# Performance work log

Hardware: AMD Instinct MI355X
Metric: run time of the kernel (lower is better)

## Reference

```python
import jax, jax.numpy as jnp
import numpy as np

B, S, D = 8, 4096, 1024
CAPACITY = 0.75
K = max(1, int(S * CAPACITY))  # 3072


def setup_inputs() -> dict:
    key = jax.random.key(0)
    k1, k2, k3 = jax.random.split(key, 3)
    x = jax.random.normal(k1, (B, S, D), dtype=jnp.float32)
    processed = jax.random.normal(k2, (B, K, D), dtype=jnp.float32)
    w_router = jax.random.normal(k3, (D,), dtype=jnp.float32) * 0.02
    return {"x": x, "processed": processed, "w_router": w_router}


def reference(x, processed, w_router):
    # --- MoDRouter.forward ---
    bsz, seq_len, dim = x.shape
    k = processed.shape[1]
    # scores: (B, S) = Linear(dim -> 1, no bias)
    scores = jnp.einsum('bsd,d->bs', x, w_router)
    # top-k per batch row, sorted descending (matches torch.topk sorted=True)
    topk_scores, indices = jax.lax.top_k(scores, k)  # (B, K)
    # gather routed tokens: (B, K, D)
    routed_x = jnp.take_along_axis(x, indices[:, :, None], axis=1)
    # --- MoDRouter.scatter_back (processed = block output for routed tokens) ---
    weights = jax.nn.softmax(topk_scores, axis=1)[:, :, None]  # (B, K, 1)
    # original values at routed positions == routed_x (same gather)
    blended = processed * weights + (1.0 - weights) * routed_x  # (B, K, D)
    batch_idx = jnp.arange(bsz)[:, None]  # (B, 1)
    output = x.at[batch_idx, indices].set(blended)  # unrouted positions keep x
    return output
```

## Files before the change

### kernel.cpp

```cpp
#include <hip/hip_runtime.h>
#include <math.h>

#define BB 8
#define SS 4096
#define DD 1024
#define KK 3072
#define NCHUNK 8
#define CHUNK 512
#define NELEM (BB * SS)

typedef unsigned long long u64;
typedef unsigned int u32;

__global__ __launch_bounds__(256) void mod_scores(const float* __restrict__ x,
                                                  const float* __restrict__ w,
                                                  float* __restrict__ scores,
                                                  u64* __restrict__ keys) {
    int wave = (int)((blockIdx.x * blockDim.x + threadIdx.x) >> 6);
    int lane = threadIdx.x & 63;
    if (wave >= NELEM) return;
    const float4* xr = (const float4*)(x + (size_t)wave * DD);
    const float4* wr = (const float4*)w;
    float acc = 0.f;
#pragma unroll
    for (int i = 0; i < 4; ++i) {
        float4 a = xr[lane + 64 * i];
        float4 b = wr[lane + 64 * i];
        acc += a.x * b.x + a.y * b.y + a.z * b.z + a.w * b.w;
    }
#pragma unroll
    for (int off = 32; off > 0; off >>= 1)
        acc += __shfl_down(acc, off, 64);
    if (lane == 0) {
        scores[wave] = acc;
        u32 u = __float_as_uint(acc);
        u32 m = (u & 0x80000000u) ? ~u : (u | 0x80000000u);
        keys[wave] = ((u64)(~m) << 32) | (u32)(wave & (SS - 1));
    }
}

__global__ __launch_bounds__(256) void mod_rank_partial(const u64* __restrict__ keys,
                                                        int* __restrict__ pcnt) {
    __shared__ __align__(16) u64 lk[CHUNK];
    const int ob = blockIdx.x / NCHUNK;
    const int c  = blockIdx.x - ob * NCHUNK;
    const int tid = threadIdx.x;
    const int gid = ob * 256 + tid;
    const int b = gid >> 12;
    const int lane = tid & 63;

    const u64* __restrict__ cand = keys + ((size_t)b << 12) + c * CHUNK;
    *(ulonglong2*)&lk[tid * 2] = *(const ulonglong2*)&cand[tid * 2];
    __syncthreads();

    const u64 my = keys[gid];
    const u32 my_hi = (u32)(my >> 32);
    const u32 my_lo = (u32)my;

    int v_cnt = 0;
#pragma unroll
    for (int g = 0; g < 8; ++g) {
        u64 mj[8];
#pragma unroll
        for (int j = 0; j < 8; ++j) {
            u32 h = (u32)__builtin_amdgcn_readlane((int)my_hi, g * 8 + j);
            u32 l = (u32)__builtin_amdgcn_readlane((int)my_lo, g * 8 + j);
            mj[j] = ((u64)h << 32) | l;
        }
        int cnt[8] = {0, 0, 0, 0, 0, 0, 0, 0};
#pragma unroll
        for (int cg = 0; cg < CHUNK / 64; ++cg) {
            u64 cv = lk[cg * 64 + lane];
#pragma unroll
            for (int j = 0; j < 8; ++j)
                cnt[j] += (int)__popcll(__ballot(cv < mj[j]));
        }
#pragma unroll
        for (int j = 0; j < 8; ++j)
            v_cnt = (lane == g * 8 + j) ? cnt[j] : v_cnt;
    }
    pcnt[c * NELEM + gid] = v_cnt;
}

__global__ __launch_bounds__(256) void mod_finalize(const int* __restrict__ pcnt,
                                                    const float* __restrict__ scores,
                                                    int* __restrict__ rank_of,
                                                    float* __restrict__ partial) {
    const int gid = blockIdx.x * 256 + threadIdx.x;
    int r = 0;
#pragma unroll
    for (int c = 0; c < NCHUNK; ++c) r += pcnt[c * NELEM + gid];
    rank_of[gid] = r;

    float e = (r < KK) ? expf(scores[gid]) : 0.f;
    __shared__ float red[256];
    red[threadIdx.x] = e;
    __syncthreads();
    for (int off = 128; off > 0; off >>= 1) {
        if (threadIdx.x < off) red[threadIdx.x] += red[threadIdx.x + off];
        __syncthreads();
    }
    if (threadIdx.x == 0) partial[blockIdx.x] = red[0];
}

__global__ __launch_bounds__(256) void mod_blend(const float* __restrict__ x,
                                                 const float* __restrict__ proc,
                                                 const int* __restrict__ rank_of,
                                                 const float* __restrict__ scores,
                                                 const float* __restrict__ partial,
                                                 float* __restrict__ out) {
    const int row = blockIdx.x;
    const int b = row >> 12;
    const int t = threadIdx.x;
    const float4* xr = (const float4*)(x + (size_t)row * DD);
    float4* orow = (float4*)(out + (size_t)row * DD);
    const int j = rank_of[row];
    float4 a = xr[t];
    if (j < KK) {
        float denom = 0.f;
#pragma unroll
        for (int i = 0; i < 16; ++i) denom += partial[b * 16 + i];
        float w = expf(scores[row]) / denom;
        const float4* pr = (const float4*)(proc + ((size_t)b * KK + j) * DD);
        float4 p = pr[t];
        float4 o;
        o.x = p.x * w + (1.f - w) * a.x;
        o.y = p.y * w + (1.f - w) * a.y;
        o.z = p.z * w + (1.f - w) * a.z;
        o.w = p.w * w + (1.f - w) * a.w;
        orow[t] = o;
    } else {
        orow[t] = a;
    }
}

extern "C" void kernel_launch(void* const* d_in, const int* in_sizes, int n_in,
                              void* d_out, int out_size, void* d_ws, size_t ws_size,
                              hipStream_t stream) {
    const float* x    = (const float*)d_in[0];
    const float* proc = (const float*)d_in[1];
    const float* w    = (const float*)d_in[2];
    float* out = (float*)d_out;

    u64*   keys    = (u64*)d_ws;
    float* scores  = (float*)((char*)d_ws + NELEM * 8);
    int*   rank_of = (int*)((char*)d_ws + NELEM * 12);
    int*   pcnt    = (int*)((char*)d_ws + NELEM * 16);
    float* partial = (float*)((char*)d_ws + NELEM * 16 + NELEM * 4 * NCHUNK);

    mod_scores      <<<NELEM / 4, 256, 0, stream>>>(x, w, scores, keys);
    mod_rank_partial<<<(NELEM / 256) * NCHUNK, 256, 0, stream>>>(keys, pcnt);
    mod_finalize    <<<NELEM / 256, 256, 0, stream>>>(pcnt, scores, rank_of, partial);
    mod_blend       <<<NELEM, 256, 0, stream>>>(x, proc, rank_of, scores, partial, out);
}
```

Baseline: 93.34 us.

## Fuse partial ranking and finalize into one full-row rank kernel, nontemporal blend

Merges the chunked rank-count kernel and the finalize/softmax-partial kernel into a single kernel where each block loads all 4096 keys of its batch row into LDS and computes full ranks directly. This removes the intermediate partial-count buffer traffic and one kernel launch. The blend kernel switches to vector-type arithmetic with nontemporal loads/stores for the streaming processed/output data. The fused rank kernel launches only 128 blocks, so it exposes much less parallelism than the previous 1024-block split.

```diff
diff --git a/kernel.cpp b/kernel.cpp
--- a/kernel.cpp
+++ b/kernel.cpp
@@ -5,12 +5,11 @@
 #define SS 4096
 #define DD 1024
 #define KK 3072
-#define NCHUNK 8
-#define CHUNK 512
 #define NELEM (BB * SS)
 
 typedef unsigned long long u64;
 typedef unsigned int u32;
+typedef float f32x4 __attribute__((ext_vector_type(4)));
 
 __global__ __launch_bounds__(256) void mod_scores(const float* __restrict__ x,
                                                   const float* __restrict__ w,
@@ -39,18 +38,24 @@
     }
 }
 
-__global__ __launch_bounds__(256) void mod_rank_partial(const u64* __restrict__ keys,
-                                                        int* __restrict__ pcnt) {
-    __shared__ __align__(16) u64 lk[CHUNK];
-    const int ob = blockIdx.x / NCHUNK;
-    const int c  = blockIdx.x - ob * NCHUNK;
+__global__ __launch_bounds__(256) void mod_rank(const u64* __restrict__ keys,
+                                                const float* __restrict__ scores,
+                                                int* __restrict__ rank_of,
+                                                float* __restrict__ partial) {
+    __shared__ __align__(16) u64 lk[SS];
+    __shared__ float red[256];
+    const int ob = blockIdx.x;
     const int tid = threadIdx.x;
     const int gid = ob * 256 + tid;
     const int b = gid >> 12;
     const int lane = tid & 63;
 
-    const u64* __restrict__ cand = keys + ((size_t)b << 12) + c * CHUNK;
-    *(ulonglong2*)&lk[tid * 2] = *(const ulonglong2*)&cand[tid * 2];
+    const u64* __restrict__ kb = keys + ((size_t)b << 12);
+#pragma unroll
+    for (int i = 0; i < 8; ++i) {
+        int idx = tid + 256 * i;
+        *(ulonglong2*)&lk[2 * idx] = *(const ulonglong2*)&kb[2 * idx];
+    }
     __syncthreads();
 
     const u64 my = keys[gid];
@@ -68,8 +73,7 @@
             mj[j] = ((u64)h << 32) | l;
         }
         int cnt[8] = {0, 0, 0, 0, 0, 0, 0, 0};
-#pragma unroll
-        for (int cg = 0; cg < CHUNK / 64; ++cg) {
+        for (int cg = 0; cg < SS / 64; ++cg) {
             u64 cv = lk[cg * 64 + lane];
 #pragma unroll
             for (int j = 0; j < 8; ++j)
@@ -79,28 +83,16 @@
         for (int j = 0; j < 8; ++j)
             v_cnt = (lane == g * 8 + j) ? cnt[j] : v_cnt;
     }
-    pcnt[c * NELEM + gid] = v_cnt;
-}
+    rank_of[gid] = v_cnt;
 
-__global__ __launch_bounds__(256) void mod_finalize(const int* __restrict__ pcnt,
-                                                    const float* __restrict__ scores,
-                                                    int* __restrict__ rank_of,
-                                                    float* __restrict__ partial) {
-    const int gid = blockIdx.x * 256 + threadIdx.x;
-    int r = 0;
-#pragma unroll
-    for (int c = 0; c < NCHUNK; ++c) r += pcnt[c * NELEM + gid];
-    rank_of[gid] = r;
-
-    float e = (r < KK) ? expf(scores[gid]) : 0.f;
-    __shared__ float red[256];
-    red[threadIdx.x] = e;
+    float e = (v_cnt < KK) ? expf(scores[gid]) : 0.f;
+    red[tid] = e;
     __syncthreads();
     for (int off = 128; off > 0; off >>= 1) {
-        if (threadIdx.x < off) red[threadIdx.x] += red[threadIdx.x + off];
+        if (tid < off) red[tid] += red[tid + off];
         __syncthreads();
     }
-    if (threadIdx.x == 0) partial[blockIdx.x] = red[0];
+    if (tid == 0) partial[ob] = red[0];
 }
 
 __global__ __launch_bounds__(256) void mod_blend(const float* __restrict__ x,
@@ -112,25 +104,21 @@
     const int row = blockIdx.x;
     const int b = row >> 12;
     const int t = threadIdx.x;
-    const float4* xr = (const float4*)(x + (size_t)row * DD);
-    float4* orow = (float4*)(out + (size_t)row * DD);
+    const f32x4* xr = (const f32x4*)(x + (size_t)row * DD);
+    f32x4* orow = (f32x4*)(out + (size_t)row * DD);
     const int j = rank_of[row];
-    float4 a = xr[t];
+    f32x4 a = xr[t];
     if (j < KK) {
         float denom = 0.f;
 #pragma unroll
         for (int i = 0; i < 16; ++i) denom += partial[b * 16 + i];
         float w = expf(scores[row]) / denom;
-        const float4* pr = (const float4*)(proc + ((size_t)b * KK + j) * DD);
-        float4 p = pr[t];
-        float4 o;
-        o.x = p.x * w + (1.f - w) * a.x;
-        o.y = p.y * w + (1.f - w) * a.y;
-        o.z = p.z * w + (1.f - w) * a.z;
-        o.w = p.w * w + (1.f - w) * a.w;
-        orow[t] = o;
+        const f32x4* pr = (const f32x4*)(proc + ((size_t)b * KK + j) * DD);
+        f32x4 p = __builtin_nontemporal_load(pr + t);
+        f32x4 o = p * w + (1.f - w) * a;
+        __builtin_nontemporal_store(o, orow + t);
     } else {
-        orow[t] = a;
+        __builtin_nontemporal_store(a, orow + t);
     }
 }
 
@@ -145,11 +133,9 @@
     u64*   keys    = (u64*)d_ws;
     float* scores  = (float*)((char*)d_ws + NELEM * 8);
     int*   rank_of = (int*)((char*)d_ws + NELEM * 12);
-    int*   pcnt    = (int*)((char*)d_ws + NELEM * 16);
-    float* partial = (float*)((char*)d_ws + NELEM * 16 + NELEM * 4 * NCHUNK);
+    float* partial = (float*)((char*)d_ws + NELEM * 16);
 
-    mod_scores      <<<NELEM / 4, 256, 0, stream>>>(x, w, scores, keys);
-    mod_rank_partial<<<(NELEM / 256) * NCHUNK, 256, 0, stream>>>(keys, pcnt);
-    mod_finalize    <<<NELEM / 256, 256, 0, stream>>>(pcnt, scores, rank_of, partial);
-    mod_blend       <<<NELEM, 256, 0, stream>>>(x, proc, rank_of, scores, partial, out);
+    mod_scores<<<NELEM / 4, 256, 0, stream>>>(x, w, scores, keys);
+    mod_rank  <<<NELEM / 256, 256, 0, stream>>>(keys, scores, rank_of, partial);
+    mod_blend <<<NELEM, 256, 0, stream>>>(x, proc, rank_of, scores, partial, out);
 }
```

Measured after the change: 113.5 us. 1.22x slower.
